# Optimization experiments

Measured on AMD Instinct MI355X. Metric: run time of the kernel, lower is better.

The kernel has to match this reference:

```python
import jax, jax.numpy as jnp
import numpy as np

DIM = 512
HEADS = 8
WIN = 64            # sqrt(num_patches) = sqrt(4096)
NUM_PATCHES = WIN * WIN
B = 8
N = 1024
NUM_REL = (2 * WIN - 1) ** 2 + 3


def _relative_position_index():
    # Same construction as RelativePositionBias.__init__ (torch meshgrid default is 'ij')
    coords = np.stack(np.meshgrid(np.arange(WIN), np.arange(WIN), indexing='ij'))  # [2,W,W]
    cf = coords.reshape(2, -1)                              # [2, W*W]
    rel = cf[:, :, None] - cf[:, None, :]                   # [2, P, P]
    rel = rel.transpose(1, 2, 0).copy()                     # [P, P, 2]
    rel[:, :, 0] += WIN - 1
    rel[:, :, 1] += WIN - 1
    rel[:, :, 0] *= 2 * WIN - 1
    return rel.sum(-1).astype(np.int32)                     # [P, P]


def setup_inputs() -> dict:
    key = jax.random.key(0)
    k_x, k_ids, k_qkv, k_proj, k_tab = jax.random.split(key, 5)
    x = jax.random.normal(k_x, (B, N, DIM), dtype=jnp.float32)
    ids_keep = jax.random.randint(k_ids, (B, N), 0, NUM_PATCHES, dtype=jnp.int32)
    w_qkv = jax.random.normal(k_qkv, (DIM, 3 * DIM), dtype=jnp.float32) * 0.02
    w_proj = jax.random.normal(k_proj, (DIM, DIM), dtype=jnp.float32) * 0.02
    b_proj = jnp.zeros((DIM,), dtype=jnp.float32)
    rel_table = jax.random.normal(k_tab, (NUM_REL, HEADS), dtype=jnp.float32) * 0.02
    rel_index = jnp.asarray(_relative_position_index())
    return {"x": x, "ids_keep": ids_keep, "w_qkv": w_qkv, "w_proj": w_proj,
            "b_proj": b_proj, "rel_table": rel_table, "rel_index": rel_index}


def reference(x, ids_keep, w_qkv, w_proj, b_proj, rel_table, rel_index):
    Bb, Nn, C = x.shape
    H = rel_table.shape[1]
    D = C // H
    # QKV projection (no bias, matching qkv_bias=False)
    qkv = (x @ w_qkv).reshape(Bb, Nn, 3, H, D).transpose(2, 0, 3, 1, 4)  # [3,B,H,N,D]
    q, k, v = qkv[0], qkv[1], qkv[2]
    # Masked relative position bias: double gather via index lookup, then table lookup.
    # Equivalent to gathering rows/cols of the full [P,P] bias with ids_keep.
    idx = rel_index[ids_keep[:, :, None], ids_keep[:, None, :]]          # [B,N,N]
    bias = rel_table[idx].transpose(0, 3, 1, 2)                          # [B,H,N,N]
    # Scaled dot-product attention with additive bias (xformers applies 1/sqrt(D))
    scale = 1.0 / jnp.sqrt(jnp.asarray(D, dtype=x.dtype))
    scores = jnp.einsum('bhnd,bhmd->bhnm', q, k) * scale + bias
    attn = jax.nn.softmax(scores, axis=-1)
    out = jnp.einsum('bhnm,bhmd->bnhd', attn, v).reshape(Bb, Nn, C)
    return out @ w_proj + b_proj
```

## Files before the change

### kernel.cpp

```cpp
#include <hip/hip_runtime.h>

typedef __attribute__((ext_vector_type(8))) __bf16 bf16x8;
typedef __attribute__((ext_vector_type(4))) float f32x4;
typedef __attribute__((ext_vector_type(16))) float f32x16;
typedef __attribute__((ext_vector_type(4))) unsigned int u32x4;
typedef unsigned short u16;
typedef unsigned int u32;

__device__ __forceinline__ u16 f2bf(float f) {
  __bf16 h = (__bf16)f;
  return *(u16*)&h;
}
__device__ __forceinline__ float bf2f(u16 h) {
  return __uint_as_float(((u32)h) << 16);
}
__device__ __forceinline__ u32 pack2(float lo, float hi) {
  return (u32)f2bf(lo) | ((u32)f2bf(hi) << 16);
}
__device__ __forceinline__ f32x4 mfma16(bf16x8 a, bf16x8 b, f32x4 c) {
  return __builtin_amdgcn_mfma_f32_16x16x32_bf16(a, b, c, 0, 0, 0);
}
__device__ __forceinline__ f32x16 mfma32(bf16x8 a, bf16x8 b, f32x16 c) {
  return __builtin_amdgcn_mfma_f32_32x32x16_bf16(a, b, c, 0, 0, 0);
}
__device__ __forceinline__ void gl16(const void* g, void* l) {
  __builtin_amdgcn_global_load_lds(
      (const __attribute__((address_space(1))) void*)g,
      (__attribute__((address_space(3))) void*)l, 16, 0, 0);
}

__global__ void cvt_to_bf16(const float* __restrict__ src, u16* __restrict__ dst, int n) {
  const int i = (blockIdx.x * 256 + threadIdx.x) * 4;
  if (i + 3 < n) {
    const float4 v = *(const float4*)(src + i);
    ushort4 o; o.x = f2bf(v.x); o.y = f2bf(v.y); o.z = f2bf(v.z); o.w = f2bf(v.w);
    *(ushort4*)(dst + i) = o;
  }
}

__global__ __launch_bounds__(256) void prep_misc(
    const float* __restrict__ w_qkv, const float* __restrict__ w_proj,
    const float* __restrict__ rel_tab,
    u16* __restrict__ wT, u16* __restrict__ wpT, u16* __restrict__ tabb)
{
  __shared__ float tile[32][33];
  const int b = blockIdx.x;
  const int tid = threadIdx.x;
  if (b < 1024) {
    const float* src; u16* dst; int C, c0, r0;
    if (b < 768) { src = w_qkv; dst = wT; C = 1536; c0 = (b % 48) * 32; r0 = (b / 48) * 32; }
    else { const int bb = b - 768; src = w_proj; dst = wpT; C = 512; c0 = (bb % 16) * 32; r0 = (bb / 16) * 32; }
    const int tx = tid & 31, ty = tid >> 5;
    for (int i = ty; i < 32; i += 8)
      tile[i][tx] = src[(size_t)(r0 + i) * C + c0 + tx];
    __syncthreads();
    for (int i = ty; i < 32; i += 8)
      dst[(size_t)(c0 + i) * 512 + r0 + tx] = f2bf(tile[tx][i]);
  } else {
    const int i = ((b - 1024) * 256 + tid) * 4;
    if (i + 3 < 16131 * 8) {
      const float4 v = *(const float4*)(rel_tab + i);
      ushort4 o; o.x = f2bf(v.x); o.y = f2bf(v.y); o.z = f2bf(v.z); o.w = f2bf(v.w);
      *(ushort4*)(tabb + i) = o;
    }
  }
}

template<int MODE>
__global__ __launch_bounds__(256, 2) void gemm_bt(
    const u16* __restrict__ A, const u16* __restrict__ Bt,
    u16* __restrict__ out0, u16* __restrict__ out1,
    float* __restrict__ fout, const float* __restrict__ bias)
{
  __shared__ u16 As[128][32];
  __shared__ u16 Bs[128][32];
  const int tid = threadIdx.x;
  const int w = tid >> 6, l = tid & 63;
  const int lr = l & 15, lg = l >> 4;
  const int wr = w >> 1, wc = w & 1;
  const int m0 = blockIdx.y * 128, n0 = blockIdx.x * 128;
  const int sl = (lr >> 1) & 3;
  const int cA = lg ^ sl;

  f32x4 acc[4][4] = {};

  for (int k0 = 0; k0 < 512; k0 += 32) {
#pragma unroll
    for (int it = 0; it < 2; ++it) {
      const int ch = it * 256 + tid;
      const int row = ch >> 2, cslot = ch & 3;
      const int csrc = cslot ^ ((row >> 1) & 3);
      gl16(A  + (size_t)(m0 + row) * 512 + k0 + csrc * 8, (u16*)As + ch * 8);
      gl16(Bt + (size_t)(n0 + row) * 512 + k0 + csrc * 8, (u16*)Bs + ch * 8);
    }
    __syncthreads();
    bf16x8 af[4], bfr[4];
#pragma unroll
    for (int mi = 0; mi < 4; ++mi)
      af[mi] = *(const bf16x8*)&As[wr * 64 + mi * 16 + lr][cA * 8];
#pragma unroll
    for (int nj = 0; nj < 4; ++nj)
      bfr[nj] = *(const bf16x8*)&Bs[wc * 64 + nj * 16 + lr][cA * 8];
#pragma unroll
    for (int mi = 0; mi < 4; ++mi)
#pragma unroll
      for (int nj = 0; nj < 4; ++nj)
        acc[mi][nj] = mfma16(af[mi], bfr[nj], acc[mi][nj]);
    __syncthreads();
  }

#pragma unroll
  for (int mi = 0; mi < 4; ++mi)
#pragma unroll
    for (int nj = 0; nj < 4; ++nj) {
      const int i0 = m0 + wr * 64 + mi * 16 + lg * 4;
      const int j  = n0 + wc * 64 + nj * 16 + lr;
      if (MODE == 0) {
        const int bb = j >> 10, n = j & 1023;
        const bool isQ = i0 < 512;
        const int f = isQ ? i0 : i0 - 512;
        const int h = f >> 6, d0 = f & 63;
        const float scl = isQ ? 0.125f : 1.0f;
        u16* dst = isQ ? out0 : out1;
        const size_t off = ((size_t)(bb * 8 + h) << 16) +
            ((((n >> 5) * 4 + (d0 >> 4)) * 2 + ((d0 >> 3) & 1)) << 8) +
            ((n & 31) << 3) + (d0 & 7);
        ushort4 o;
        o.x = f2bf(acc[mi][nj][0] * scl); o.y = f2bf(acc[mi][nj][1] * scl);
        o.z = f2bf(acc[mi][nj][2] * scl); o.w = f2bf(acc[mi][nj][3] * scl);
        *(ushort4*)(dst + off) = o;
      } else if (MODE == 1) {
        const int bb = i0 >> 10, m = i0 & 1023;
        const int h = j >> 6, d = j & 63;
        const size_t off = ((size_t)(bb * 8 + h) << 16) +
            ((((m >> 6) * 4 + ((m >> 4) & 3)) * 2 + ((m >> 2) & 1)) << 9) +
            (d << 3) + (((m >> 3) & 1) << 2);
        ushort4 o;
        o.x = f2bf(acc[mi][nj][0]); o.y = f2bf(acc[mi][nj][1]);
        o.z = f2bf(acc[mi][nj][2]); o.w = f2bf(acc[mi][nj][3]);
        *(ushort4*)(out0 + off) = o;
      } else {
        const float4 bp = *(const float4*)(bias + i0);
        float4 o;
        o.x = acc[mi][nj][0] + bp.x; o.y = acc[mi][nj][1] + bp.y;
        o.z = acc[mi][nj][2] + bp.z; o.w = acc[mi][nj][3] + bp.w;
        *(float4*)(fout + (size_t)j * 512 + i0) = o;
      }
    }
}

__global__ __launch_bounds__(512, 2) void flash_attn(
    const u16* __restrict__ Qs, const u16* __restrict__ Ks,
    const u16* __restrict__ Vs, const int* __restrict__ ids_keep,
    const u16* __restrict__ tab_bf,
    u16* __restrict__ attn_out)
{
  __shared__ u16 tabL[16129 * 4];
  __shared__ int bofs[1024];

  const int bid = blockIdx.x;
  const int bb = bid & 7;
  const int r2 = bid >> 3;
  const int hp = r2 & 1;
  const int g64 = r2 >> 1;
  const int tid = threadIdx.x;
  const int wv = tid >> 6;
  const int hloc = wv & 3;
  const int qs = wv >> 2;
  const int l = tid & 63, l31 = l & 31, hi5 = l >> 5;
  const int h = hp * 4 + hloc;

  for (int e = tid; e < 16129; e += 512)
    *(ushort4*)&tabL[e * 4] = *(const ushort4*)(tab_bf + (size_t)e * 8 + hp * 4);
  for (int e = tid; e < 1024; e += 512) {
    const int id = ids_keep[bb * 1024 + e];
    bofs[e] = (8064 - ((id >> 6) * 127 + (id & 63))) * 8;
  }

  const int nloc = g64 * 64 + qs * 32 + l31;
  const int idn = ids_keep[bb * 1024 + nloc];
  const int base = ((idn >> 6) * 127 + (idn & 63)) * 8 + hloc * 2;

  const size_t hb = (size_t)(bb * 8 + h) << 16;
  const int g32 = g64 * 2 + qs;

  f32x16 acc0 = {}, acc1 = {};
  float lsum = 0.f;

  bf16x8 qf[4];
#pragma unroll
  for (int dch = 0; dch < 4; ++dch)
    qf[dch] = *(const bf16x8*)(Qs + hb + (size_t)(((g32 * 4 + dch) * 2 + hi5) * 256 + l31 * 8));

  auto kload = [&](int t, bf16x8 (&kf)[8]) {
#pragma unroll
    for (int u = 0; u < 2; ++u)
#pragma unroll
      for (int dch = 0; dch < 4; ++dch)
        kf[u * 4 + dch] = *(const bf16x8*)(Ks + hb +
            (size_t)((((2 * t + u) * 4 + dch) * 2 + hi5) * 256 + l31 * 8));
  };
  auto vload = [&](int t, bf16x8 (&vf)[8]) {
#pragma unroll
    for (int cp = 0; cp < 4; ++cp)
#pragma unroll
      for (int dc = 0; dc < 2; ++dc)
        vf[cp * 2 + dc] = *(const bf16x8*)(Vs + hb +
            (size_t)(((t * 4 + cp) * 2 + hi5) * 512 + (dc * 32 + l31) * 8));
  };

  __syncthreads();

  bf16x8 kA[8], kB[8], vA[8], vB[8];
  kload(0, kA);
  vload(0, vA);

  const char* tb = (const char*)tabL;

  auto body = [&](int t, bool pf, bf16x8 (&kC)[8], bf16x8 (&kN)[8],
                  bf16x8 (&vC)[8], bf16x8 (&vN)[8]) {
    if (pf) {
      kload(t + 1, kN);
      vload(t + 1, vN);
    }

    u32 pk[2][4][2];
#pragma unroll
    for (int u = 0; u < 2; ++u) {
      f32x16 s = {};
      s = mfma32(kC[u * 4 + 0], qf[0], s);
      s = mfma32(kC[u * 4 + 1], qf[1], s);
      s = mfma32(kC[u * 4 + 2], qf[2], s);
      s = mfma32(kC[u * 4 + 3], qf[3], s);
#pragma unroll
      for (int a = 0; a < 4; ++a) {
        const int4 bo = *(const int4*)&bofs[t * 64 + u * 32 + a * 8 + hi5 * 4];
        const float b0 = bf2f(*(const u16*)(tb + base + bo.x));
        const float b1 = bf2f(*(const u16*)(tb + base + bo.y));
        const float b2 = bf2f(*(const u16*)(tb + base + bo.z));
        const float b3 = bf2f(*(const u16*)(tb + base + bo.w));
        float p0 = __expf(s[a * 4 + 0] + b0);
        float p1 = __expf(s[a * 4 + 1] + b1);
        float p2 = __expf(s[a * 4 + 2] + b2);
        float p3 = __expf(s[a * 4 + 3] + b3);
        lsum += (p0 + p1) + (p2 + p3);
        pk[u][a][0] = pack2(p0, p1);
        pk[u][a][1] = pack2(p2, p3);
      }
    }

#pragma unroll
    for (int cp = 0; cp < 4; ++cp) {
      const int u = cp >> 1, cc = cp & 1;
      union { u32x4 u4; bf16x8 v; } pb;
      pb.u4 = (u32x4){pk[u][2 * cc][0], pk[u][2 * cc][1],
                      pk[u][2 * cc + 1][0], pk[u][2 * cc + 1][1]};
      acc0 = mfma32(vC[cp * 2 + 0], pb.v, acc0);
      acc1 = mfma32(vC[cp * 2 + 1], pb.v, acc1);
    }
  };

  for (int tt = 0; tt < 16; tt += 2) {
    body(tt,     tt < 15,     kA, kB, vA, vB);
    body(tt + 1, tt + 1 < 15, kB, kA, vB, vA);
  }

  lsum += __shfl_xor(lsum, 32);
  const float inv = 1.0f / lsum;
  const int nglob = bb * 1024 + nloc;
#pragma unroll
  for (int dc = 0; dc < 2; ++dc) {
    const f32x16& av = dc ? acc1 : acc0;
#pragma unroll
    for (int rq = 0; rq < 4; ++rq) {
      const int d = dc * 32 + rq * 8 + hi5 * 4;
      ushort4 o;
      o.x = f2bf(av[rq * 4 + 0] * inv);
      o.y = f2bf(av[rq * 4 + 1] * inv);
      o.z = f2bf(av[rq * 4 + 2] * inv);
      o.w = f2bf(av[rq * 4 + 3] * inv);
      *(ushort4*)(attn_out + (size_t)nglob * 512 + h * 64 + d) = o;
    }
  }
}

extern "C" void kernel_launch(void* const* d_in, const int* in_sizes, int n_in,
                              void* d_out, int out_size, void* d_ws, size_t ws_size,
                              hipStream_t stream) {
  const float* x        = (const float*)d_in[0];
  const int*   ids      = (const int*)d_in[1];
  const float* w_qkv    = (const float*)d_in[2];
  const float* w_proj   = (const float*)d_in[3];
  const float* b_proj   = (const float*)d_in[4];
  const float* rel_tab  = (const float*)d_in[5];
  float* out = (float*)d_out;

  char* ws = (char*)d_ws;
  u16* xb   = (u16*)(ws);
  u16* wT   = (u16*)(ws + 8388608);
  u16* wpT  = (u16*)(ws + 9961472);
  u16* Qsw  = (u16*)(ws + 10485760);
  u16* Ksw  = (u16*)(ws + 18874368);
  u16* Vsw  = (u16*)(ws + 27262976);
  u16* tabb = (u16*)(ws + 35651584);
  u16* attn = xb;

  cvt_to_bf16<<<4096, 256, 0, stream>>>(x, xb, 8 * 1024 * 512);
  prep_misc<<<1151, 256, 0, stream>>>(w_qkv, w_proj, rel_tab, wT, wpT, tabb);

  gemm_bt<0><<<dim3(64, 8), 256, 0, stream>>>(wT, xb, Qsw, Ksw, nullptr, nullptr);
  gemm_bt<1><<<dim3(4, 64), 256, 0, stream>>>(xb, wT + 1024 * 512, Vsw, nullptr, nullptr, nullptr);

  flash_attn<<<dim3(256), 512, 0, stream>>>(Qsw, Ksw, Vsw, ids, tabb, attn);

  gemm_bt<2><<<dim3(64, 4), 256, 0, stream>>>(wpT, attn, nullptr, nullptr, out, b_proj);
}
```

Baseline: 96.21 us.

## Split attention KV range across two wave groups with LDS combine

The attention kernel doubles its block to 1024 threads. Each half processes eight of the sixteen KV tiles for the same queries and heads, and the partial accumulators and row sums are merged through shared memory aliased over the bias table. The K/V register double-buffered prefetch is dropped in favour of direct loads inside the loop. The aim is more waves per block to hide latency on a grid of only 256 blocks. The cost is an extra LDS combine, an extra barrier, and losing the explicit prefetch pipeline.

After: 94.50 us (median of 2 runs). No clear change (-1.8%).

```diff
diff --git a/kernel.cpp b/kernel.cpp
--- a/kernel.cpp
+++ b/kernel.cpp
@@ -149,13 +149,16 @@
     }
 }
 
-__global__ __launch_bounds__(512, 2) void flash_attn(
+__global__ __launch_bounds__(1024) void flash_attn(
     const u16* __restrict__ Qs, const u16* __restrict__ Ks,
     const u16* __restrict__ Vs, const int* __restrict__ ids_keep,
     const u16* __restrict__ tab_bf,
     u16* __restrict__ attn_out)
 {
-  __shared__ u16 tabL[16129 * 4];
+  __shared__ union {
+    u16 tabL[16129 * 4];
+    float comb[8][33][64];
+  } sm;
   __shared__ int bofs[1024];
 
   const int bid = blockIdx.x;
@@ -166,15 +169,17 @@
   const int tid = threadIdx.x;
   const int wv = tid >> 6;
   const int hloc = wv & 3;
-  const int qs = wv >> 2;
+  const int qs = (wv >> 2) & 1;
+  const int kvh = wv >> 3;
   const int l = tid & 63, l31 = l & 31, hi5 = l >> 5;
   const int h = hp * 4 + hloc;
-
-  for (int e = tid; e < 16129; e += 512)
-    *(ushort4*)&tabL[e * 4] = *(const ushort4*)(tab_bf + (size_t)e * 8 + hp * 4);
-  for (int e = tid; e < 1024; e += 512) {
-    const int id = ids_keep[bb * 1024 + e];
-    bofs[e] = (8064 - ((id >> 6) * 127 + (id & 63))) * 8;
+  const int t0 = kvh * 8;
+
+  for (int e = tid; e < 16129; e += 1024)
+    *(ushort4*)&sm.tabL[e * 4] = *(const ushort4*)(tab_bf + (size_t)e * 8 + hp * 4);
+  {
+    const int id = ids_keep[bb * 1024 + tid];
+    bofs[tid] = (8064 - ((id >> 6) * 127 + (id & 63))) * 8;
   }
 
   const int nloc = g64 * 64 + qs * 32 + l31;
@@ -192,46 +197,24 @@
   for (int dch = 0; dch < 4; ++dch)
     qf[dch] = *(const bf16x8*)(Qs + hb + (size_t)(((g32 * 4 + dch) * 2 + hi5) * 256 + l31 * 8));
 
-  auto kload = [&](int t, bf16x8 (&kf)[8]) {
-#pragma unroll
-    for (int u = 0; u < 2; ++u)
+  __syncthreads();
+
+  const char* tb = (const char*)sm.tabL;
+
+  for (int t = t0; t < t0 + 8; ++t) {
+    u32 pk[2][4][2];
+#pragma unroll
+    for (int u = 0; u < 2; ++u) {
+      bf16x8 kc[4];
 #pragma unroll
       for (int dch = 0; dch < 4; ++dch)
-        kf[u * 4 + dch] = *(const bf16x8*)(Ks + hb +
+        kc[dch] = *(const bf16x8*)(Ks + hb +
             (size_t)((((2 * t + u) * 4 + dch) * 2 + hi5) * 256 + l31 * 8));
-  };
-  auto vload = [&](int t, bf16x8 (&vf)[8]) {
-#pragma unroll
-    for (int cp = 0; cp < 4; ++cp)
-#pragma unroll
-      for (int dc = 0; dc < 2; ++dc)
-        vf[cp * 2 + dc] = *(const bf16x8*)(Vs + hb +
-            (size_t)(((t * 4 + cp) * 2 + hi5) * 512 + (dc * 32 + l31) * 8));
-  };
-
-  __syncthreads();
-
-  bf16x8 kA[8], kB[8], vA[8], vB[8];
-  kload(0, kA);
-  vload(0, vA);
-
-  const char* tb = (const char*)tabL;
-
-  auto body = [&](int t, bool pf, bf16x8 (&kC)[8], bf16x8 (&kN)[8],
-                  bf16x8 (&vC)[8], bf16x8 (&vN)[8]) {
-    if (pf) {
-      kload(t + 1, kN);
-      vload(t + 1, vN);
-    }
-
-    u32 pk[2][4][2];
-#pragma unroll
-    for (int u = 0; u < 2; ++u) {
       f32x16 s = {};
-      s = mfma32(kC[u * 4 + 0], qf[0], s);
-      s = mfma32(kC[u * 4 + 1], qf[1], s);
-      s = mfma32(kC[u * 4 + 2], qf[2], s);
-      s = mfma32(kC[u * 4 + 3], qf[3], s);
+      s = mfma32(kc[0], qf[0], s);
+      s = mfma32(kc[1], qf[1], s);
+      s = mfma32(kc[2], qf[2], s);
+      s = mfma32(kc[3], qf[3], s);
 #pragma unroll
       for (int a = 0; a < 4; ++a) {
         const int4 bo = *(const int4*)&bofs[t * 64 + u * 32 + a * 8 + hi5 * 4];
@@ -251,35 +234,48 @@
 
 #pragma unroll
     for (int cp = 0; cp < 4; ++cp) {
+      bf16x8 vc[2];
+#pragma unroll
+      for (int dc = 0; dc < 2; ++dc)
+        vc[dc] = *(const bf16x8*)(Vs + hb +
+            (size_t)(((t * 4 + cp) * 2 + hi5) * 512 + (dc * 32 + l31) * 8));
       const int u = cp >> 1, cc = cp & 1;
       union { u32x4 u4; bf16x8 v; } pb;
       pb.u4 = (u32x4){pk[u][2 * cc][0], pk[u][2 * cc][1],
                       pk[u][2 * cc + 1][0], pk[u][2 * cc + 1][1]};
-      acc0 = mfma32(vC[cp * 2 + 0], pb.v, acc0);
-      acc1 = mfma32(vC[cp * 2 + 1], pb.v, acc1);
-    }
-  };
-
-  for (int tt = 0; tt < 16; tt += 2) {
-    body(tt,     tt < 15,     kA, kB, vA, vB);
-    body(tt + 1, tt + 1 < 15, kB, kA, vB, vA);
+      acc0 = mfma32(vc[0], pb.v, acc0);
+      acc1 = mfma32(vc[1], pb.v, acc1);
+    }
   }
 
   lsum += __shfl_xor(lsum, 32);
-  const float inv = 1.0f / lsum;
-  const int nglob = bb * 1024 + nloc;
-#pragma unroll
-  for (int dc = 0; dc < 2; ++dc) {
-    const f32x16& av = dc ? acc1 : acc0;
-#pragma unroll
-    for (int rq = 0; rq < 4; ++rq) {
-      const int d = dc * 32 + rq * 8 + hi5 * 4;
-      ushort4 o;
-      o.x = f2bf(av[rq * 4 + 0] * inv);
-      o.y = f2bf(av[rq * 4 + 1] * inv);
-      o.z = f2bf(av[rq * 4 + 2] * inv);
-      o.w = f2bf(av[rq * 4 + 3] * inv);
-      *(ushort4*)(attn_out + (size_t)nglob * 512 + h * 64 + d) = o;
+
+  __syncthreads();
+  const int slot = wv & 7;
+  if (kvh == 1) {
+#pragma unroll
+    for (int r = 0; r < 16; ++r) sm.comb[slot][r][l]      = acc0[r];
+#pragma unroll
+    for (int r = 0; r < 16; ++r) sm.comb[slot][16 + r][l] = acc1[r];
+    sm.comb[slot][32][l] = lsum;
+  }
+  __syncthreads();
+  if (kvh == 0) {
+    const float inv = 1.0f / (lsum + sm.comb[slot][32][l]);
+    const int nglob = bb * 1024 + nloc;
+#pragma unroll
+    for (int dc = 0; dc < 2; ++dc) {
+      const f32x16& av = dc ? acc1 : acc0;
+#pragma unroll
+      for (int rq = 0; rq < 4; ++rq) {
+        const int d = dc * 32 + rq * 8 + hi5 * 4;
+        ushort4 o;
+        o.x = f2bf((av[rq * 4 + 0] + sm.comb[slot][dc * 16 + rq * 4 + 0][l]) * inv);
+        o.y = f2bf((av[rq * 4 + 1] + sm.comb[slot][dc * 16 + rq * 4 + 1][l]) * inv);
+        o.z = f2bf((av[rq * 4 + 2] + sm.comb[slot][dc * 16 + rq * 4 + 2][l]) * inv);
+        o.w = f2bf((av[rq * 4 + 3] + sm.comb[slot][dc * 16 + rq * 4 + 3][l]) * inv);
+        *(ushort4*)(attn_out + (size_t)nglob * 512 + h * 64 + d) = o;
+      }
     }
   }
 }
@@ -311,7 +307,7 @@
   gemm_bt<0><<<dim3(64, 8), 256, 0, stream>>>(wT, xb, Qsw, Ksw, nullptr, nullptr);
   gemm_bt<1><<<dim3(4, 64), 256, 0, stream>>>(xb, wT + 1024 * 512, Vsw, nullptr, nullptr, nullptr);
 
-  flash_attn<<<dim3(256), 512, 0, stream>>>(Qsw, Ksw, Vsw, ids, tabb, attn);
+  flash_attn<<<dim3(256), 1024, 0, stream>>>(Qsw, Ksw, Vsw, ids, tabb, attn);
 
   gemm_bt<2><<<dim3(64, 4), 256, 0, stream>>>(wpT, attn, nullptr, nullptr, out, b_proj);
 }
```
